# Optimization experiments

Hardware: AMD Instinct MI355X
Metric: run time of the kernel (lower is better)

The kernel has to match this reference:

```python
import jax, jax.numpy as jnp
import numpy as np

B, N, D = 4, 2048, 2048
HEADS, KV_HEADS = 16, 4
DH = D // HEADS            # 128 per-head dim
KV_RATIO = HEADS // KV_HEADS
MAX_LEN, MAX_BSZ = 2048, 4
EPS = 1.1920929e-07        # torch.finfo(float32).eps (RMSNorm default eps=None)


def _rot_tables(n, d, base=10000.0):
    thetas = base ** (-jnp.arange(0, d, 2, dtype=jnp.float32) / d)   # [d/2]
    ang = jnp.arange(n, dtype=jnp.float32)[:, None] * thetas[None, :]
    cos = jnp.repeat(jnp.cos(ang), 2, axis=-1)   # [n, d] interleaved pairs
    sin = jnp.repeat(jnp.sin(ang), 2, axis=-1)
    return cos, sin


def _rotate_half_inverted(x):
    x1 = x[..., ::2]
    x2 = x[..., 1::2]
    return jnp.stack([-x2, x1], axis=-1).reshape(x.shape)


def _apply_rotation(x, end, start=0):
    cos, sin = _rot_tables(MAX_LEN, DH)
    return x * cos[start:end] + _rotate_half_inverted(x) * sin[start:end]


def setup_inputs() -> dict:
    key = jax.random.key(0)
    ks = jax.random.split(key, 4)
    s = 0.02
    return {
        "x": jax.random.normal(ks[0], (B, N, D), jnp.float32),
        "norm_w": jnp.ones((D,), jnp.float32),
        "qw": jax.random.normal(ks[1], (HEADS * DH, D), jnp.float32) * s,
        "qb": jnp.zeros((HEADS * DH,), jnp.float32),
        "kvw": jax.random.normal(ks[2], (2 * DH * KV_HEADS, D), jnp.float32) * s,
        "kvb": jnp.zeros((2 * DH * KV_HEADS,), jnp.float32),
        "wow": jax.random.normal(ks[3], (D, HEADS * DH), jnp.float32) * s,
        "wob": jnp.zeros((D,), jnp.float32),
        "kv_cache": jnp.zeros((MAX_BSZ, MAX_LEN, 2 * DH * KV_HEADS), jnp.float32),
        "pos": 0,
    }


def reference(x, norm_w, qw, qb, kvw, kvb, wow, wob, kv_cache, pos):
    b, n, d = x.shape
    t = pos + n  # total cached length
    # RMSNorm
    xn = x * jax.lax.rsqrt(jnp.mean(x * x, axis=-1, keepdims=True) + EPS) * norm_w
    # Q projection -> [b, heads, n, dh]
    q = (xn @ qw.T + qb).reshape(b, n, HEADS, DH).transpose(0, 2, 1, 3)
    # KV projection + cache write/read
    kv = xn @ kvw.T + kvb                                  # [b, n, 2*dh*kv_heads]
    cache = jax.lax.dynamic_update_slice(kv_cache, kv, (0, pos, 0))
    kvf = cache[:b, :t].reshape(b, t, KV_HEADS, 2 * DH).transpose(0, 2, 1, 3)
    kvf = jnp.repeat(kvf, KV_RATIO, axis=1)                # GQA expand -> [b, heads, t, 2dh]
    k, v = kvf[..., :DH], kvf[..., DH:]
    # RoPE (interleaved-pair variant)
    q = _apply_rotation(q, t, pos)
    k = _apply_rotation(k, t, 0)
    # Attention (decoder causal)
    attn = jnp.einsum("bhqd,bhkd->bhqk", q, k) / jnp.sqrt(jnp.float32(DH))
    if n > 1:
        mask = jnp.triu(jnp.ones((n, t), bool), k=1 + pos)
        attn = jnp.where(mask, -jnp.inf, attn)
    attn = jax.nn.softmax(attn, axis=-1)
    o = jnp.einsum("bhqk,bhkd->bhqd", attn, v).transpose(0, 2, 1, 3).reshape(b, n, HEADS * DH)
    return o @ wow.T + wob
```

## Files before the change

kernel.cpp:

```cpp
#include <hip/hip_runtime.h>
#include <hip/hip_bf16.h>

typedef unsigned short u16;
typedef unsigned int u32;
typedef __attribute__((ext_vector_type(4))) float f32x4;
typedef __attribute__((ext_vector_type(8))) short s16x8;

#define B_ 4
#define N_ 2048
#define D_ 2048
#define HEADS_ 16
#define KVH_ 4
#define DH_ 128
#define KVD_ 1024
#define M_ 8192
#define SCALE_ 0.08838834764831845f
#define QSCALE2_ 0.12753257518622628f

__device__ __forceinline__ u16 f2bf(float f) {
  u32 u = __builtin_bit_cast(u32, f);
  return (u16)((u + 0x7FFFu + ((u >> 16) & 1u)) >> 16);
}

__device__ __forceinline__ float fexp2(float x) {
#if __has_builtin(__builtin_amdgcn_exp2f)
  return __builtin_amdgcn_exp2f(x);
#else
  return exp2f(x);
#endif
}

__device__ __forceinline__ void gload_lds16(const void* g, void* l) {
  __builtin_amdgcn_global_load_lds(
      (const __attribute__((address_space(1))) u32*)g,
      (__attribute__((address_space(3))) u32*)l, 16, 0, 0);
}

__global__ __launch_bounds__(256)
void rope_tab_k(float* __restrict__ cost, float* __restrict__ sint)
{
  const int idx = blockIdx.x * 256 + threadIdx.x;
  const int p = idx >> 6, i = idx & 63;
  const float theta = expf(-(float)i * 0.015625f * 9.210340371976184f);
  float s, c;
  sincosf((float)p * theta, &s, &c);
  cost[idx] = c;
  sint[idx] = s;
}

__global__ __launch_bounds__(256)
void cvt_bf16_k(const float* __restrict__ s, u16* __restrict__ d, int n)
{
  const int i = (blockIdx.x * 256 + threadIdx.x) * 8;
  if (i >= n) return;
  const f32x4 a = *(const f32x4*)(s + i);
  const f32x4 b = *(const f32x4*)(s + i + 4);
  s16x8 o;
  #pragma unroll
  for (int j = 0; j < 4; ++j) { o[j] = (short)f2bf(a[j]); o[4 + j] = (short)f2bf(b[j]); }
  *(s16x8*)(d + i) = o;
}

__global__ __launch_bounds__(256)
void rmsnorm_k(const float* __restrict__ x, const float* __restrict__ w, u16* __restrict__ xn)
{
  const int row = blockIdx.x, t = threadIdx.x;
  const float* xr = x + (size_t)row * D_;
  const f32x4 a = *(const f32x4*)(xr + t * 8);
  const f32x4 b = *(const f32x4*)(xr + t * 8 + 4);
  float ss = a[0]*a[0] + a[1]*a[1] + a[2]*a[2] + a[3]*a[3]
           + b[0]*b[0] + b[1]*b[1] + b[2]*b[2] + b[3]*b[3];
  #pragma unroll
  for (int off = 32; off >= 1; off >>= 1) ss += __shfl_xor(ss, off);
  __shared__ float wss[4];
  if ((t & 63) == 0) wss[t >> 6] = ss;
  __syncthreads();
  const float tot = wss[0] + wss[1] + wss[2] + wss[3];
  const float rs = rsqrtf(tot * (1.0f / D_) + 1.1920929e-07f);
  s16x8 o;
  #pragma unroll
  for (int j = 0; j < 4; ++j) {
    o[j]     = (short)f2bf(a[j] * rs * w[t * 8 + j]);
    o[4 + j] = (short)f2bf(b[j] * rs * w[t * 8 + 4 + j]);
  }
  *(s16x8*)(xn + (size_t)row * D_ + t * 8) = o;
}

template<int EPI>
__global__ __launch_bounds__(256)
void gemm_bt(const u16* __restrict__ A, const u16* __restrict__ Bw,
             void* __restrict__ Cv, void* __restrict__ Cv2,
             const float* __restrict__ bias, const float* __restrict__ bias2,
             int N, int K,
             const float* __restrict__ cos_t, const float* __restrict__ sin_t)
{
  __shared__ u16 As[128 * 32];
  __shared__ u16 Bs[128 * 32];
  const int t = threadIdx.x;
  const int w = t >> 6, lane = t & 63;
  const int g = lane >> 4, lr = lane & 15;
  const int row0 = blockIdx.x * 128, col0 = blockIdx.y * 128;
  const int wr = (w >> 1) * 64, wc = (w & 1) * 64;

  f32x4 acc[4][4] = {};

  const u16* gA = A + (size_t)(row0 + w * 16 + (lane >> 2)) * K + (lane & 3) * 8;
  const u16* gB = Bw + (size_t)(col0 + w * 16 + (lane >> 2)) * K + (lane & 3) * 8;
  u16* lA = As + (w * 16) * 32;
  u16* lB = Bs + (w * 16) * 32;

  for (int kt = 0; kt < K; kt += 32) {
    #pragma unroll
    for (int r = 0; r < 2; ++r) {
      gload_lds16(gA + (size_t)(r * 64) * K + kt, lA + r * 64 * 32);
      gload_lds16(gB + (size_t)(r * 64) * K + kt, lB + r * 64 * 32);
    }
    __syncthreads();
    s16x8 af[4], bf[4];
    #pragma unroll
    for (int i = 0; i < 4; ++i) {
      af[i] = *(const s16x8*)(As + (wr + i * 16 + lr) * 32 + g * 8);
      bf[i] = *(const s16x8*)(Bs + (wc + i * 16 + lr) * 32 + g * 8);
    }
    #pragma unroll
    for (int mi = 0; mi < 4; ++mi)
      #pragma unroll
      for (int ni = 0; ni < 4; ++ni)
        acc[mi][ni] = __builtin_amdgcn_mfma_f32_16x16x32_bf16(af[mi], bf[ni], acc[mi][ni], 0, 0, 0);
    __syncthreads();
  }

  #pragma unroll
  for (int mi = 0; mi < 4; ++mi) {
    #pragma unroll
    for (int ni = 0; ni < 4; ++ni) {
      const int cc = col0 + wc + ni * 16 + lr;
      const float bv = (EPI == 4 && cc >= 2048) ? bias2[cc - 2048] : bias[cc];
      #pragma unroll
      for (int j = 0; j < 4; ++j) {
        const int rr = row0 + wr + mi * 16 + g * 4 + j;
        float v = acc[mi][ni][j] + bv;
        if (EPI == 0) {
          ((float*)Cv)[(size_t)rr * 2048 + cc] = v;
        } else {
          const int pos = rr & (N_ - 1);
          const float pv = __shfl_xor(v, 1);
          if (cc < 2048) {
            const int d = cc & (DH_ - 1);
            const float c = cos_t[pos * 64 + (d >> 1)];
            const float s = sin_t[pos * 64 + (d >> 1)];
            const float o = (cc & 1) ? fmaf(v, c, pv * s) : fmaf(v, c, -pv * s);
            ((u16*)Cv)[(size_t)rr * 2048 + cc] = f2bf(o);
          } else {
            const int ccc = cc - 2048;
            const int dm = ccc & 255;
            float o = v;
            if (dm < DH_) {
              const float c = cos_t[pos * 64 + (dm >> 1)];
              const float s = sin_t[pos * 64 + (dm >> 1)];
              o = (dm & 1) ? fmaf(v, c, pv * s) : fmaf(v, c, -pv * s);
            }
            ((u16*)Cv2)[(size_t)rr * 1024 + ccc] = f2bf(o);
          }
        }
      }
    }
  }
}

__global__ __launch_bounds__(256)
void vtrans_k(const u16* __restrict__ kvb, u16* __restrict__ vt)
{
  __shared__ u16 tile[64][65];
  const int z = blockIdx.z, b = z >> 2, kh = z & 3;
  const int p0 = blockIdx.x * 64, d0 = blockIdx.y * 64;
  const int t = threadIdx.x;
  #pragma unroll
  for (int r = 0; r < 2; ++r) {
    const int pl = r * 32 + (t >> 3), dl = (t & 7) * 8;
    const s16x8 v = *(const s16x8*)(kvb + (size_t)(b * N_ + p0 + pl) * KVD_ + kh * 256 + 128 + d0 + dl);
    #pragma unroll
    for (int jj = 0; jj < 8; ++jj) tile[pl][dl + jj] = (u16)v[jj];
  }
  __syncthreads();
  #pragma unroll
  for (int r = 0; r < 2; ++r) {
    const int dl = r * 32 + (t >> 3), pl = (t & 7) * 8;
    s16x8 o;
    #pragma unroll
    for (int jj = 0; jj < 8; ++jj) o[jj] = (short)tile[pl + jj][dl];
    *(s16x8*)(vt + ((size_t)(z * DH_ + d0 + dl)) * N_ + p0 + pl) = o;
  }
}

__global__ __launch_bounds__(512, 2)
void attn_k(const u16* __restrict__ q, const u16* __restrict__ kvb,
            const u16* __restrict__ vt, u16* __restrict__ out)
{
  const int fi = blockIdx.x, h = blockIdx.y, b = blockIdx.z;
  const int kh = h >> 2;
  const int t = threadIdx.x, w = t >> 6, lane = t & 63;
  const int g = lane >> 4, lr = lane & 15;

  __shared__ __align__(16) u16 Ks[2][64 * 128];
  __shared__ __align__(16) u16 Vs[2][128 * 64];
  __shared__ __align__(16) u16 Ps[8][16 * 64];

  const int kc = 2 * w;
  const int kr0 = kc * 4 + (lane >> 4);
  const int ksw0 = (lane & 15) ^ (kr0 & 7);
  const int kr1 = kr0 + 4;
  const int ksw1 = (lane & 15) ^ (kr1 & 7);
  const int vd0 = kc * 8 + (lane >> 3);
  const int vsw0 = (lane & 7) ^ (vd0 & 7);
  const int vd1 = vd0 + 8;
  const int vsw1 = (lane & 7) ^ (vd1 & 7);

  const u16* kbase = kvb + (size_t)b * (N_ * KVD_) + kh * 256;
  const u16* vbase = vt + (size_t)((b * KVH_ + kh) * DH_) * N_;

  int cur = 0;

  auto issue = [&](int kt, int buf) {
    gload_lds16(kbase + (size_t)(kt * 64 + kr0) * KVD_ + ksw0 * 8, &Ks[buf][kc * 512]);
    gload_lds16(kbase + (size_t)(kt * 64 + kr1) * KVD_ + ksw1 * 8, &Ks[buf][(kc + 1) * 512]);
    gload_lds16(vbase + (size_t)vd0 * N_ + kt * 64 + vsw0 * 8, &Vs[buf][kc * 512]);
    gload_lds16(vbase + (size_t)vd1 * N_ + kt * 64 + vsw1 * 8, &Vs[buf][(kc + 1) * 512]);
  };

  auto run_qtile = [&](int qi, int nkt, bool chain) {
    const int qrow0 = qi * 128 + w * 16;
    const int td = qrow0 >> 6;
    s16x8 qf[4];
    {
      const u16* qp = q + (size_t)(b * N_ + qrow0 + lr) * D_ + h * DH_;
      #pragma unroll
      for (int ks = 0; ks < 4; ++ks) qf[ks] = *(const s16x8*)(qp + ks * 32 + g * 8);
    }
    f32x4 o_acc[8] = {};
    float m_j[4], l_j[4];
    #pragma unroll
    for (int j = 0; j < 4; ++j) { m_j[j] = -1e30f; l_j[j] = 0.0f; }

    for (int kt = 0; kt < nkt; ++kt) {
      __syncthreads();
      if (kt + 1 < nkt)      issue(kt + 1, cur ^ 1);
      else if (chain)        issue(0, cur ^ 1);

      if (kt <= td) {
        const u16* Kc = &Ks[cur][0];
        const u16* Vc = &Vs[cur][0];

        f32x4 sf[4] = {};
        __builtin_amdgcn_s_setprio(1);
        #pragma unroll
        for (int ks = 0; ks < 4; ++ks) {
          #pragma unroll
          for (int kvf = 0; kvf < 4; ++kvf) {
            const int kvr = kvf * 16 + lr;
            const int ba = (kvr * 256 + ks * 64 + g * 16) ^ ((kvr & 7) << 4);
            const s16x8 kf = *(const s16x8*)((const char*)Kc + ba);
            sf[kvf] = __builtin_amdgcn_mfma_f32_16x16x32_bf16(qf[ks], kf, sf[kvf], 0, 0, 0);
          }
        }
        __builtin_amdgcn_s_setprio(0);

        const bool need_mask = (kt == td);
        float pmax[4];
        #pragma unroll
        for (int j = 0; j < 4; ++j) {
          float mx = -1e30f;
          #pragma unroll
          for (int kvf = 0; kvf < 4; ++kvf) {
            float sv = sf[kvf][j] * QSCALE2_;
            if (need_mask) {
              const int kj = kt * 64 + kvf * 16 + lr;
              const int qi_row = qrow0 + g * 4 + j;
              if (kj > qi_row) sv = -1e30f;
            }
            sf[kvf][j] = sv;
            mx = fmaxf(mx, sv);
          }
          mx = fmaxf(mx, __shfl_xor(mx, 1));
          mx = fmaxf(mx, __shfl_xor(mx, 2));
          mx = fmaxf(mx, __shfl_xor(mx, 4));
          mx = fmaxf(mx, __shfl_xor(mx, 8));
          pmax[j] = mx;
        }

        const float needv = fmaxf(fmaxf(pmax[0] - m_j[0], pmax[1] - m_j[1]),
                                  fmaxf(pmax[2] - m_j[2], pmax[3] - m_j[3]));
        if (__any(needv > 8.0f)) {
          #pragma unroll
          for (int j = 0; j < 4; ++j) {
            const float mn = fmaxf(m_j[j], pmax[j]);
            const float pf = fexp2(m_j[j] - mn);
            m_j[j] = mn;
            l_j[j] *= pf;
            #pragma unroll
            for (int df = 0; df < 8; ++df) o_acc[df][j] *= pf;
          }
        }

        #pragma unroll
        for (int j = 0; j < 4; ++j) {
          float lacc = 0.0f;
          #pragma unroll
          for (int kvf = 0; kvf < 4; ++kvf) {
            const float p = fexp2(sf[kvf][j] - m_j[j]);
            lacc += p;
            const int rq = g * 4 + j, ck = kvf * 16 + lr;
            const int ba = (rq * 128 + ck * 2) ^ ((rq & 7) << 4);
            *(u16*)((char*)&Ps[w][0] + ba) = (u16)(__builtin_bit_cast(u32, p) >> 16);
          }
          l_j[j] += lacc;
        }

        __builtin_amdgcn_s_setprio(1);
        #pragma unroll
        for (int kk = 0; kk < 2; ++kk) {
          const int bap = (lr * 128 + kk * 64 + g * 16) ^ ((lr & 7) << 4);
          const s16x8 pf = *(const s16x8*)((const char*)&Ps[w][0] + bap);
          #pragma unroll
          for (int df = 0; df < 8; ++df) {
            const int dd = df * 16 + lr;
            const int bav = (dd * 128 + kk * 64 + g * 16) ^ ((dd & 7) << 4);
            const s16x8 vf = *(const s16x8*)((const char*)Vc + bav);
            o_acc[df] = __builtin_amdgcn_mfma_f32_16x16x32_bf16(pf, vf, o_acc[df], 0, 0, 0);
          }
        }
        __builtin_amdgcn_s_setprio(0);
      }
      cur ^= 1;
    }

    float inv_l[4];
    #pragma unroll
    for (int j = 0; j < 4; ++j) {
      float s4 = l_j[j];
      s4 += __shfl_xor(s4, 1);
      s4 += __shfl_xor(s4, 2);
      s4 += __shfl_xor(s4, 4);
      s4 += __shfl_xor(s4, 8);
      inv_l[j] = 1.0f / s4;
    }
    u16* op = out + (size_t)(b * N_ + qrow0) * D_ + h * DH_;
    #pragma unroll
    for (int df = 0; df < 8; ++df)
      #pragma unroll
      for (int j = 0; j < 4; ++j)
        op[(size_t)(g * 4 + j) * D_ + df * 16 + lr] = f2bf(o_acc[df][j] * inv_l[j]);
  };

  const int qlo = fi, qhi = 15 - fi;
  issue(0, 0);
  run_qtile(qlo, 2 * qlo + 2, true);
  run_qtile(qhi, 2 * qhi + 2, false);
}

extern "C" void kernel_launch(void* const* d_in, const int* in_sizes, int n_in,
                              void* d_out, int out_size, void* d_ws, size_t ws_size,
                              hipStream_t stream) {
  const float* x      = (const float*)d_in[0];
  const float* normw  = (const float*)d_in[1];
  const float* qw     = (const float*)d_in[2];
  const float* qbias  = (const float*)d_in[3];
  const float* kvw    = (const float*)d_in[4];
  const float* kvbias = (const float*)d_in[5];
  const float* wow    = (const float*)d_in[6];
  const float* wob    = (const float*)d_in[7];
  float* out = (float*)d_out;

  char* ws = (char*)d_ws;
  u16* xn    = (u16*)(ws + 0);
  u16* dq    = (u16*)(ws + 33554432);
  u16* dkv   = (u16*)(ws + 67108864);
  u16* dvt   = (u16*)(ws + 83886080);
  u16* wqkv  = (u16*)(ws + 92274688);
  u16* wowb  = (u16*)(ws + 104857600);
  float* cost = (float*)(ws + 113246208);
  float* sint = (float*)(ws + 113770496);

  rope_tab_k<<<512, 256, 0, stream>>>(cost, sint);
  cvt_bf16_k<<<2048, 256, 0, stream>>>(qw, wqkv, 2048 * 2048);
  cvt_bf16_k<<<1024, 256, 0, stream>>>(kvw, wqkv + 2048 * 2048, 1024 * 2048);
  cvt_bf16_k<<<2048, 256, 0, stream>>>(wow, wowb, 2048 * 2048);
  rmsnorm_k<<<8192, 256, 0, stream>>>(x, normw, xn);
  gemm_bt<4><<<dim3(64, 24), 256, 0, stream>>>(xn, wqkv, (void*)dq, (void*)dkv,
                                               qbias, kvbias, 3072, 2048, cost, sint);
  vtrans_k<<<dim3(32, 2, 16), 256, 0, stream>>>(dkv, dvt);
  attn_k<<<dim3(8, 16, 4), 512, 0, stream>>>(dq, dkv, dvt, xn);
  gemm_bt<0><<<dim3(64, 16), 256, 0, stream>>>(xn, wowb, (void*)out, nullptr,
                                               wob, nullptr, 2048, 2048, nullptr, nullptr);
}
```

Before: 461.6 us.

## Replace GEMM with 256x256-tile double-buffered kernel using swizzled LDS

Replaces the 128x128, K=32 single-buffered GEMM with a 256x256 tile, K=64, 512-thread kernel. It double-buffers LDS with staged async global-to-LDS loads interleaved across four MFMA sub-phases, and XOR-swizzles the LDS layout to avoid bank conflicts. It also raises wave priority around MFMA bursts. The aim is more data reuse per loaded byte and loads hidden behind compute, at the cost of heavy LDS use (128KB), one block per CU, and fewer blocks (384/256) on a 256-CU device, which risks tail underutilisation.

```diff
diff --git a/kernel.cpp b/kernel.cpp
--- a/kernel.cpp
+++ b/kernel.cpp
@@ -87,59 +87,135 @@
 }
 
 template<int EPI>
-__global__ __launch_bounds__(256)
-void gemm_bt(const u16* __restrict__ A, const u16* __restrict__ Bw,
+__global__ __launch_bounds__(512, 1)
+void gemm256(const u16* __restrict__ A, const u16* __restrict__ Bw,
              void* __restrict__ Cv, void* __restrict__ Cv2,
              const float* __restrict__ bias, const float* __restrict__ bias2,
-             int N, int K,
              const float* __restrict__ cos_t, const float* __restrict__ sin_t)
 {
-  __shared__ u16 As[128 * 32];
-  __shared__ u16 Bs[128 * 32];
-  const int t = threadIdx.x;
-  const int w = t >> 6, lane = t & 63;
-  const int g = lane >> 4, lr = lane & 15;
-  const int row0 = blockIdx.x * 128, col0 = blockIdx.y * 128;
-  const int wr = (w >> 1) * 64, wc = (w & 1) * 64;
-
-  f32x4 acc[4][4] = {};
-
-  const u16* gA = A + (size_t)(row0 + w * 16 + (lane >> 2)) * K + (lane & 3) * 8;
-  const u16* gB = Bw + (size_t)(col0 + w * 16 + (lane >> 2)) * K + (lane & 3) * 8;
-  u16* lA = As + (w * 16) * 32;
-  u16* lB = Bs + (w * 16) * 32;
-
-  for (int kt = 0; kt < K; kt += 32) {
-    #pragma unroll
-    for (int r = 0; r < 2; ++r) {
-      gload_lds16(gA + (size_t)(r * 64) * K + kt, lA + r * 64 * 32);
-      gload_lds16(gB + (size_t)(r * 64) * K + kt, lB + r * 64 * 32);
-    }
-    __syncthreads();
-    s16x8 af[4], bf[4];
-    #pragma unroll
-    for (int i = 0; i < 4; ++i) {
-      af[i] = *(const s16x8*)(As + (wr + i * 16 + lr) * 32 + g * 8);
-      bf[i] = *(const s16x8*)(Bs + (wc + i * 16 + lr) * 32 + g * 8);
-    }
-    #pragma unroll
-    for (int mi = 0; mi < 4; ++mi)
-      #pragma unroll
-      for (int ni = 0; ni < 4; ++ni)
-        acc[mi][ni] = __builtin_amdgcn_mfma_f32_16x16x32_bf16(af[mi], bf[ni], acc[mi][ni], 0, 0, 0);
-    __syncthreads();
+  __shared__ __align__(16) u16 As[2][16384];
+  __shared__ __align__(16) u16 Bs[2][16384];
+  const int t = threadIdx.x, w = t >> 6, l = t & 63;
+  const int g = l >> 4, lr = l & 15;
+  const int wm = w >> 2, wn = w & 3;
+  const int row0 = blockIdx.y * 256, col0 = blockIdx.x * 256;
+  const int NT = 2048 / 64;
+
+  const int sr = l >> 3;
+  const int sc = ((l & 7) * 8) ^ (sr << 3);
+  const u16* gA = A  + (size_t)(row0 + w * 8 + sr) * 2048 + sc;
+  const u16* gB = Bw + (size_t)(col0 + w * 8 + sr) * 2048 + sc;
+
+  f32x4 acc[8][4] = {};
+
+  auto stage = [&](int kt2, int q, int pb) {
+    gload_lds16(gA + (size_t)(q * 64) * 2048 + kt2 * 64, &As[pb][(q * 8 + w) * 512]);
+    gload_lds16(gB + (size_t)(q * 64) * 2048 + kt2 * 64, &Bs[pb][(q * 8 + w) * 512]);
+  };
+  auto ldf = [&](const u16* base, int row, int ks) -> s16x8 {
+    const int ba = row * 128 + ((ks * 64 + g * 16) ^ ((lr & 7) << 4));
+    return *(const s16x8*)((const char*)base + ba);
+  };
+
+  #pragma unroll
+  for (int q = 0; q < 4; ++q) stage(0, q, 0);
+
+  for (int kt = 0; kt < NT; ++kt) {
+    const int p = kt & 1, pn = p ^ 1;
+    const bool hn = (kt + 1 < NT);
+    const u16* Ap = &As[p][0];
+    const u16* Bp = &Bs[p][0];
+    s16x8 a0[4][2], b0[2][2], b1[2][2];
+
+    if (hn) { stage(kt + 1, 0, pn); asm volatile("s_waitcnt vmcnt(2)" ::: "memory"); }
+    else    {                        asm volatile("s_waitcnt vmcnt(0)" ::: "memory"); }
+    __builtin_amdgcn_s_barrier();
+    #pragma unroll
+    for (int mf = 0; mf < 4; ++mf)
+      #pragma unroll
+      for (int ks = 0; ks < 2; ++ks) a0[mf][ks] = ldf(Ap, wm * 128 + mf * 16 + lr, ks);
+    #pragma unroll
+    for (int nf = 0; nf < 2; ++nf)
+      #pragma unroll
+      for (int ks = 0; ks < 2; ++ks) b0[nf][ks] = ldf(Bp, wn * 64 + nf * 16 + lr, ks);
+    __builtin_amdgcn_s_setprio(1);
+    #pragma unroll
+    for (int mf = 0; mf < 4; ++mf)
+      #pragma unroll
+      for (int nf = 0; nf < 2; ++nf)
+        #pragma unroll
+        for (int ks = 0; ks < 2; ++ks)
+          acc[mf][nf] = __builtin_amdgcn_mfma_f32_16x16x32_bf16(a0[mf][ks], b0[nf][ks], acc[mf][nf], 0, 0, 0);
+    __builtin_amdgcn_s_setprio(0);
+    __builtin_amdgcn_sched_barrier(0);
+    __builtin_amdgcn_s_barrier();
+
+    if (hn) stage(kt + 1, 1, pn);
+    #pragma unroll
+    for (int nf = 0; nf < 2; ++nf)
+      #pragma unroll
+      for (int ks = 0; ks < 2; ++ks) b1[nf][ks] = ldf(Bp, wn * 64 + (2 + nf) * 16 + lr, ks);
+    __builtin_amdgcn_s_setprio(1);
+    #pragma unroll
+    for (int mf = 0; mf < 4; ++mf)
+      #pragma unroll
+      for (int nf = 0; nf < 2; ++nf)
+        #pragma unroll
+        for (int ks = 0; ks < 2; ++ks)
+          acc[mf][2 + nf] = __builtin_amdgcn_mfma_f32_16x16x32_bf16(a0[mf][ks], b1[nf][ks], acc[mf][2 + nf], 0, 0, 0);
+    __builtin_amdgcn_s_setprio(0);
+    __builtin_amdgcn_sched_barrier(0);
+    __builtin_amdgcn_s_barrier();
+
+    if (hn) stage(kt + 1, 2, pn);
+    #pragma unroll
+    for (int mf = 0; mf < 4; ++mf)
+      #pragma unroll
+      for (int ks = 0; ks < 2; ++ks) a0[mf][ks] = ldf(Ap, wm * 128 + (4 + mf) * 16 + lr, ks);
+    #pragma unroll
+    for (int nf = 0; nf < 2; ++nf)
+      #pragma unroll
+      for (int ks = 0; ks < 2; ++ks) b0[nf][ks] = ldf(Bp, wn * 64 + nf * 16 + lr, ks);
+    __builtin_amdgcn_s_setprio(1);
+    #pragma unroll
+    for (int mf = 0; mf < 4; ++mf)
+      #pragma unroll
+      for (int nf = 0; nf < 2; ++nf)
+        #pragma unroll
+        for (int ks = 0; ks < 2; ++ks)
+          acc[4 + mf][nf] = __builtin_amdgcn_mfma_f32_16x16x32_bf16(a0[mf][ks], b0[nf][ks], acc[4 + mf][nf], 0, 0, 0);
+    __builtin_amdgcn_s_setprio(0);
+    __builtin_amdgcn_sched_barrier(0);
+    __builtin_amdgcn_s_barrier();
+
+    if (hn) stage(kt + 1, 3, pn);
+    #pragma unroll
+    for (int nf = 0; nf < 2; ++nf)
+      #pragma unroll
+      for (int ks = 0; ks < 2; ++ks) b1[nf][ks] = ldf(Bp, wn * 64 + (2 + nf) * 16 + lr, ks);
+    __builtin_amdgcn_s_setprio(1);
+    #pragma unroll
+    for (int mf = 0; mf < 4; ++mf)
+      #pragma unroll
+      for (int nf = 0; nf < 2; ++nf)
+        #pragma unroll
+        for (int ks = 0; ks < 2; ++ks)
+          acc[4 + mf][2 + nf] = __builtin_amdgcn_mfma_f32_16x16x32_bf16(a0[mf][ks], b1[nf][ks], acc[4 + mf][2 + nf], 0, 0, 0);
+    __builtin_amdgcn_s_setprio(0);
+    __builtin_amdgcn_sched_barrier(0);
+    __builtin_amdgcn_s_barrier();
   }
 
   #pragma unroll
-  for (int mi = 0; mi < 4; ++mi) {
-    #pragma unroll
-    for (int ni = 0; ni < 4; ++ni) {
-      const int cc = col0 + wc + ni * 16 + lr;
+  for (int mf = 0; mf < 8; ++mf) {
+    #pragma unroll
+    for (int nf = 0; nf < 4; ++nf) {
+      const int cc = col0 + wn * 64 + nf * 16 + lr;
       const float bv = (EPI == 4 && cc >= 2048) ? bias2[cc - 2048] : bias[cc];
       #pragma unroll
       for (int j = 0; j < 4; ++j) {
-        const int rr = row0 + wr + mi * 16 + g * 4 + j;
-        float v = acc[mi][ni][j] + bv;
+        const int rr = row0 + wm * 128 + mf * 16 + g * 4 + j;
+        float v = acc[mf][nf][j] + bv;
         if (EPI == 0) {
           ((float*)Cv)[(size_t)rr * 2048 + cc] = v;
         } else {
@@ -386,10 +462,10 @@
   cvt_bf16_k<<<1024, 256, 0, stream>>>(kvw, wqkv + 2048 * 2048, 1024 * 2048);
   cvt_bf16_k<<<2048, 256, 0, stream>>>(wow, wowb, 2048 * 2048);
   rmsnorm_k<<<8192, 256, 0, stream>>>(x, normw, xn);
-  gemm_bt<4><<<dim3(64, 24), 256, 0, stream>>>(xn, wqkv, (void*)dq, (void*)dkv,
-                                               qbias, kvbias, 3072, 2048, cost, sint);
+  gemm256<4><<<dim3(12, 32), 512, 0, stream>>>(xn, wqkv, (void*)dq, (void*)dkv,
+                                               qbias, kvbias, cost, sint);
   vtrans_k<<<dim3(32, 2, 16), 256, 0, stream>>>(dkv, dvt);
   attn_k<<<dim3(8, 16, 4), 512, 0, stream>>>(dq, dkv, dvt, xn);
-  gemm_bt<0><<<dim3(64, 16), 256, 0, stream>>>(xn, wowb, (void*)out, nullptr,
-                                               wob, nullptr, 2048, 2048, nullptr, nullptr);
-}
+  gemm256<0><<<dim3(8, 32), 512, 0, stream>>>(xn, wowb, (void*)out, nullptr,
+                                              wob, nullptr, nullptr, nullptr);
+}
```

Result: slower. 539.4 us (+16.9%).

## Replace output projection with 256x256-tile double-buffered direct-to-LDS GEMM

Applied to the files above, without the earlier changes.

Adds a new gemm256 kernel for the output projection. It uses 256x256 block tiles, 512 threads, double-buffered global-to-LDS loads with a swizzled layout, and raised wave priority around the MFMA sections. The old gemm_bt EPI==0 path is dropped and its epilogue is simplified to always do the RoPE path. This aims to raise data reuse and overlap loads with compute for the 8192x2048x2048 projection, at the cost of only 256 blocks, one block per CU and high register pressure.

```diff
diff --git a/kernel.cpp b/kernel.cpp
--- a/kernel.cpp
+++ b/kernel.cpp
@@ -135,34 +135,125 @@
     #pragma unroll
     for (int ni = 0; ni < 4; ++ni) {
       const int cc = col0 + wc + ni * 16 + lr;
-      const float bv = (EPI == 4 && cc >= 2048) ? bias2[cc - 2048] : bias[cc];
+      const float bv = (cc >= 2048) ? bias2[cc - 2048] : bias[cc];
       #pragma unroll
       for (int j = 0; j < 4; ++j) {
         const int rr = row0 + wr + mi * 16 + g * 4 + j;
         float v = acc[mi][ni][j] + bv;
-        if (EPI == 0) {
-          ((float*)Cv)[(size_t)rr * 2048 + cc] = v;
+        const int pos = rr & (N_ - 1);
+        const float pv = __shfl_xor(v, 1);
+        if (cc < 2048) {
+          const int d = cc & (DH_ - 1);
+          const float c = cos_t[pos * 64 + (d >> 1)];
+          const float s = sin_t[pos * 64 + (d >> 1)];
+          const float o = (cc & 1) ? fmaf(v, c, pv * s) : fmaf(v, c, -pv * s);
+          ((u16*)Cv)[(size_t)rr * 2048 + cc] = f2bf(o);
         } else {
-          const int pos = rr & (N_ - 1);
-          const float pv = __shfl_xor(v, 1);
-          if (cc < 2048) {
-            const int d = cc & (DH_ - 1);
-            const float c = cos_t[pos * 64 + (d >> 1)];
-            const float s = sin_t[pos * 64 + (d >> 1)];
-            const float o = (cc & 1) ? fmaf(v, c, pv * s) : fmaf(v, c, -pv * s);
-            ((u16*)Cv)[(size_t)rr * 2048 + cc] = f2bf(o);
-          } else {
-            const int ccc = cc - 2048;
-            const int dm = ccc & 255;
-            float o = v;
-            if (dm < DH_) {
-              const float c = cos_t[pos * 64 + (dm >> 1)];
-              const float s = sin_t[pos * 64 + (dm >> 1)];
-              o = (dm & 1) ? fmaf(v, c, pv * s) : fmaf(v, c, -pv * s);
-            }
-            ((u16*)Cv2)[(size_t)rr * 1024 + ccc] = f2bf(o);
-          }
-        }
+          const int ccc = cc - 2048;
+          const int dm = ccc & 255;
+          float o = v;
+          if (dm < DH_) {
+            const float c = cos_t[pos * 64 + (dm >> 1)];
+            const float s = sin_t[pos * 64 + (dm >> 1)];
+            o = (dm & 1) ? fmaf(v, c, pv * s) : fmaf(v, c, -pv * s);
+          }
+          ((u16*)Cv2)[(size_t)rr * 1024 + ccc] = f2bf(o);
+        }
+      }
+    }
+  }
+}
+
+__global__ __launch_bounds__(512, 1)
+void gemm256(const u16* __restrict__ A, const u16* __restrict__ Bw,
+             float* __restrict__ Cv, const float* __restrict__ bias)
+{
+  __shared__ __align__(16) u16 As[2][16384];
+  __shared__ __align__(16) u16 Bs[2][16384];
+  const int t = threadIdx.x, w = t >> 6, l = t & 63;
+  const int g = l >> 4, lr = l & 15;
+  const int wm = w >> 2, wn = w & 3;
+  const int row0 = blockIdx.y * 256, col0 = blockIdx.x * 256;
+  const int NT = 2048 / 64;
+
+  const int sr = l >> 3;
+  const int sc = ((l & 7) * 8) ^ (sr << 3);
+  const u16* gA = A  + (size_t)(row0 + w * 8 + sr) * 2048 + sc;
+  const u16* gB = Bw + (size_t)(col0 + w * 8 + sr) * 2048 + sc;
+
+  f32x4 acc[8][4] = {};
+
+  auto stage_tile = [&](int kt2, int pb) {
+    #pragma unroll
+    for (int q = 0; q < 4; ++q) {
+      gload_lds16(gA + (size_t)(q * 64) * 2048 + kt2 * 64, &As[pb][(q * 8 + w) * 512]);
+      gload_lds16(gB + (size_t)(q * 64) * 2048 + kt2 * 64, &Bs[pb][(q * 8 + w) * 512]);
+    }
+  };
+  auto ldf = [&](const u16* base, int row, int ks) -> s16x8 {
+    const int ba = row * 128 + ((ks * 64 + g * 16) ^ ((lr & 7) << 4));
+    return *(const s16x8*)((const char*)base + ba);
+  };
+
+  stage_tile(0, 0);
+
+  for (int kt = 0; kt < NT; ++kt) {
+    const int p = kt & 1;
+    if (kt + 1 < NT) {
+      stage_tile(kt + 1, p ^ 1);
+      asm volatile("s_waitcnt vmcnt(8)" ::: "memory");
+    } else {
+      asm volatile("s_waitcnt vmcnt(0)" ::: "memory");
+    }
+    __builtin_amdgcn_s_barrier();
+
+    const u16* Ap = &As[p][0];
+    const u16* Bp = &Bs[p][0];
+    s16x8 af[4][2], bf[4][2];
+    #pragma unroll
+    for (int nf = 0; nf < 4; ++nf)
+      #pragma unroll
+      for (int ks = 0; ks < 2; ++ks) bf[nf][ks] = ldf(Bp, wn * 64 + nf * 16 + lr, ks);
+    #pragma unroll
+    for (int mf = 0; mf < 4; ++mf)
+      #pragma unroll
+      for (int ks = 0; ks < 2; ++ks) af[mf][ks] = ldf(Ap, wm * 128 + mf * 16 + lr, ks);
+    __builtin_amdgcn_s_setprio(1);
+    #pragma unroll
+    for (int mf = 0; mf < 4; ++mf)
+      #pragma unroll
+      for (int nf = 0; nf < 4; ++nf)
+        #pragma unroll
+        for (int ks = 0; ks < 2; ++ks)
+          acc[mf][nf] = __builtin_amdgcn_mfma_f32_16x16x32_bf16(af[mf][ks], bf[nf][ks], acc[mf][nf], 0, 0, 0);
+    __builtin_amdgcn_s_setprio(0);
+    #pragma unroll
+    for (int mf = 0; mf < 4; ++mf)
+      #pragma unroll
+      for (int ks = 0; ks < 2; ++ks) af[mf][ks] = ldf(Ap, wm * 128 + (4 + mf) * 16 + lr, ks);
+    __builtin_amdgcn_s_setprio(1);
+    #pragma unroll
+    for (int mf = 0; mf < 4; ++mf)
+      #pragma unroll
+      for (int nf = 0; nf < 4; ++nf)
+        #pragma unroll
+        for (int ks = 0; ks < 2; ++ks)
+          acc[4 + mf][nf] = __builtin_amdgcn_mfma_f32_16x16x32_bf16(af[mf][ks], bf[nf][ks], acc[4 + mf][nf], 0, 0, 0);
+    __builtin_amdgcn_s_setprio(0);
+    __builtin_amdgcn_sched_barrier(0);
+    __builtin_amdgcn_s_barrier();
+  }
+
+  #pragma unroll
+  for (int mf = 0; mf < 8; ++mf) {
+    #pragma unroll
+    for (int nf = 0; nf < 4; ++nf) {
+      const int cc = col0 + wn * 64 + nf * 16 + lr;
+      const float bv = bias[cc];
+      #pragma unroll
+      for (int j = 0; j < 4; ++j) {
+        const int rr = row0 + wm * 128 + mf * 16 + g * 4 + j;
+        Cv[(size_t)rr * 2048 + cc] = acc[mf][nf][j] + bv;
       }
     }
   }
@@ -390,6 +481,5 @@
                                                qbias, kvbias, 3072, 2048, cost, sint);
   vtrans_k<<<dim3(32, 2, 16), 256, 0, stream>>>(dkv, dvt);
   attn_k<<<dim3(8, 16, 4), 512, 0, stream>>>(dq, dkv, dvt, xn);
-  gemm_bt<0><<<dim3(64, 16), 256, 0, stream>>>(xn, wowb, (void*)out, nullptr,
-                                               wob, nullptr, 2048, 2048, nullptr, nullptr);
-}
+  gemm256<<<dim3(8, 32), 512, 0, stream>>>(xn, wowb, out, wob);
+}
```

New measurement: 431.0 us. 6.6% less time.

## Double-buffer GEMM with 256x128 tiles, 512 threads and swizzled block order

Applied to the files above, without the earlier changes.

Replaces the single-buffered 128x128 GEMM with a 256x128-tile, 8-wave kernel that double-buffers LDS. The next K-tile is prefetched with global_load_lds while MFMAs run on the current one, using explicit vmcnt waits and raw barriers. It also raises priority around the MFMA block and remaps block indices for L2 locality. The aim is to hide global-load latency and cut barrier stalls in both projection GEMMs. The cost is more LDS per block and higher register pressure.

```diff
diff --git a/kernel.cpp b/kernel.cpp
--- a/kernel.cpp
+++ b/kernel.cpp
@@ -14,7 +14,6 @@
 #define DH_ 128
 #define KVD_ 1024
 #define M_ 8192
-#define SCALE_ 0.08838834764831845f
 #define QSCALE2_ 0.12753257518622628f
 
 __device__ __forceinline__ u16 f2bf(float f) {
@@ -87,59 +86,80 @@
 }
 
 template<int EPI>
-__global__ __launch_bounds__(256)
-void gemm_bt(const u16* __restrict__ A, const u16* __restrict__ Bw,
-             void* __restrict__ Cv, void* __restrict__ Cv2,
-             const float* __restrict__ bias, const float* __restrict__ bias2,
-             int N, int K,
-             const float* __restrict__ cos_t, const float* __restrict__ sin_t)
-{
-  __shared__ u16 As[128 * 32];
-  __shared__ u16 Bs[128 * 32];
-  const int t = threadIdx.x;
-  const int w = t >> 6, lane = t & 63;
-  const int g = lane >> 4, lr = lane & 15;
-  const int row0 = blockIdx.x * 128, col0 = blockIdx.y * 128;
-  const int wr = (w >> 1) * 64, wc = (w & 1) * 64;
-
-  f32x4 acc[4][4] = {};
-
-  const u16* gA = A + (size_t)(row0 + w * 16 + (lane >> 2)) * K + (lane & 3) * 8;
-  const u16* gB = Bw + (size_t)(col0 + w * 16 + (lane >> 2)) * K + (lane & 3) * 8;
-  u16* lA = As + (w * 16) * 32;
-  u16* lB = Bs + (w * 16) * 32;
-
-  for (int kt = 0; kt < K; kt += 32) {
-    #pragma unroll
-    for (int r = 0; r < 2; ++r) {
-      gload_lds16(gA + (size_t)(r * 64) * K + kt, lA + r * 64 * 32);
-      gload_lds16(gB + (size_t)(r * 64) * K + kt, lB + r * 64 * 32);
+__global__ __launch_bounds__(512, 2)
+void gemm_p(const u16* __restrict__ A, const u16* __restrict__ Bw,
+            void* __restrict__ Cv, void* __restrict__ Cv2,
+            const float* __restrict__ bias, const float* __restrict__ bias2,
+            const float* __restrict__ cos_t, const float* __restrict__ sin_t)
+{
+  __shared__ __align__(16) u16 As[2][8192];
+  __shared__ __align__(16) u16 Bs[2][4096];
+  const int t = threadIdx.x, w = t >> 6, l = t & 63;
+  const int g = l >> 4, lr = l & 15;
+  const int wm = w >> 2, wn = w & 3;
+
+  const int nbx = gridDim.x;
+  const int nb = nbx * gridDim.y;
+  const int flat = blockIdx.y * nbx + blockIdx.x;
+  const int swz = (flat & 7) * (nb >> 3) + (flat >> 3);
+  const int row0 = (swz / nbx) * 256, col0 = (swz % nbx) * 128;
+
+  const int NT = 64;
+
+  const int srow = w * 16 + (l >> 2);
+  const int scol = (l & 3) * 8;
+  const u16* gA = A + (size_t)(row0 + srow) * 2048 + scol;
+  const u16* gB = Bw + (size_t)(col0 + srow) * 2048 + scol;
+
+  f32x4 acc[8][2] = {};
+
+  auto stage_tile = [&](int kt2, int pb) {
+    gload_lds16(gA + (size_t)kt2 * 32, &As[pb][(w * 16) * 32]);
+    gload_lds16(gA + (size_t)128 * 2048 + kt2 * 32, &As[pb][(128 + w * 16) * 32]);
+    gload_lds16(gB + (size_t)kt2 * 32, &Bs[pb][(w * 16) * 32]);
+  };
+
+  stage_tile(0, 0);
+
+  for (int kt = 0; kt < NT; ++kt) {
+    const int p = kt & 1;
+    if (kt + 1 < NT) {
+      stage_tile(kt + 1, p ^ 1);
+      asm volatile("s_waitcnt vmcnt(3)" ::: "memory");
+    } else {
+      asm volatile("s_waitcnt vmcnt(0)" ::: "memory");
     }
-    __syncthreads();
-    s16x8 af[4], bf[4];
-    #pragma unroll
-    for (int i = 0; i < 4; ++i) {
-      af[i] = *(const s16x8*)(As + (wr + i * 16 + lr) * 32 + g * 8);
-      bf[i] = *(const s16x8*)(Bs + (wc + i * 16 + lr) * 32 + g * 8);
-    }
-    #pragma unroll
-    for (int mi = 0; mi < 4; ++mi)
+    __builtin_amdgcn_s_barrier();
+
+    s16x8 bf[2], af[8];
+    #pragma unroll
+    for (int nf = 0; nf < 2; ++nf)
+      bf[nf] = *(const s16x8*)(&Bs[p][(wn * 32 + nf * 16 + lr) * 32 + g * 8]);
+    #pragma unroll
+    for (int mf = 0; mf < 8; ++mf)
+      af[mf] = *(const s16x8*)(&As[p][(wm * 128 + mf * 16 + lr) * 32 + g * 8]);
+
+    __builtin_amdgcn_s_setprio(1);
+    #pragma unroll
+    for (int mf = 0; mf < 8; ++mf)
       #pragma unroll
-      for (int ni = 0; ni < 4; ++ni)
-        acc[mi][ni] = __builtin_amdgcn_mfma_f32_16x16x32_bf16(af[mi], bf[ni], acc[mi][ni], 0, 0, 0);
-    __syncthreads();
+      for (int nf = 0; nf < 2; ++nf)
+        acc[mf][nf] = __builtin_amdgcn_mfma_f32_16x16x32_bf16(af[mf], bf[nf], acc[mf][nf], 0, 0, 0);
+    __builtin_amdgcn_s_setprio(0);
+    __builtin_amdgcn_sched_barrier(0);
+    __builtin_amdgcn_s_barrier();
   }
 
   #pragma unroll
-  for (int mi = 0; mi < 4; ++mi) {
-    #pragma unroll
-    for (int ni = 0; ni < 4; ++ni) {
-      const int cc = col0 + wc + ni * 16 + lr;
+  for (int mf = 0; mf < 8; ++mf) {
+    #pragma unroll
+    for (int nf = 0; nf < 2; ++nf) {
+      const int cc = col0 + wn * 32 + nf * 16 + lr;
       const float bv = (EPI == 4 && cc >= 2048) ? bias2[cc - 2048] : bias[cc];
       #pragma unroll
       for (int j = 0; j < 4; ++j) {
-        const int rr = row0 + wr + mi * 16 + g * 4 + j;
-        float v = acc[mi][ni][j] + bv;
+        const int rr = row0 + wm * 128 + mf * 16 + g * 4 + j;
+        float v = acc[mf][nf][j] + bv;
         if (EPI == 0) {
           ((float*)Cv)[(size_t)rr * 2048 + cc] = v;
         } else {
@@ -386,10 +406,10 @@
   cvt_bf16_k<<<1024, 256, 0, stream>>>(kvw, wqkv + 2048 * 2048, 1024 * 2048);
   cvt_bf16_k<<<2048, 256, 0, stream>>>(wow, wowb, 2048 * 2048);
   rmsnorm_k<<<8192, 256, 0, stream>>>(x, normw, xn);
-  gemm_bt<4><<<dim3(64, 24), 256, 0, stream>>>(xn, wqkv, (void*)dq, (void*)dkv,
-                                               qbias, kvbias, 3072, 2048, cost, sint);
+  gemm_p<4><<<dim3(24, 32), 512, 0, stream>>>(xn, wqkv, (void*)dq, (void*)dkv,
+                                              qbias, kvbias, cost, sint);
   vtrans_k<<<dim3(32, 2, 16), 256, 0, stream>>>(dkv, dvt);
   attn_k<<<dim3(8, 16, 4), 512, 0, stream>>>(dq, dkv, dvt, xn);
-  gemm_bt<0><<<dim3(64, 16), 256, 0, stream>>>(xn, wowb, (void*)out, nullptr,
-                                               wob, nullptr, 2048, 2048, nullptr, nullptr);
-}
+  gemm_p<0><<<dim3(16, 32), 512, 0, stream>>>(xn, wowb, (void*)out, nullptr,
+                                              wob, nullptr, nullptr, nullptr);
+}
```

After: 423.1 us. 1.09x faster.
